# Performance work log

Hardware: AMD Instinct MI355X
Metric: run time of the kernel (lower is better)

The kernel has to match this reference:

```python
import jax, jax.numpy as jnp
import numpy as np

B, T, E = 8, 2048, 512   # batch, tokens, embedding_dim
K, C = 8192, 8           # num_embeddings, codebook_dim
LN_EPS = 1e-5


def _layer_norm(x, g, b):
    mu = jnp.mean(x, axis=-1, keepdims=True)
    var = jnp.var(x, axis=-1, keepdims=True)
    return (x - mu) * jax.lax.rsqrt(var + LN_EPS) * g + b


def setup_inputs() -> dict:
    key = jax.random.key(0)
    ks = jax.random.split(key, 8)
    s_e = 1.0 / np.sqrt(E)
    s_c = 1.0 / np.sqrt(C)
    return {
        "features": jax.random.normal(ks[0], (B, T, E), dtype=jnp.float32),
        # project_in: Linear(E,E) -> ReLU -> Linear(E,C)
        "W1_in": jax.random.uniform(ks[1], (E, E), jnp.float32, -s_e, s_e),
        "b1_in": jnp.zeros((E,), jnp.float32),
        "W2_in": jax.random.uniform(ks[2], (E, C), jnp.float32, -s_e, s_e),
        "b2_in": jnp.zeros((C,), jnp.float32),
        "ln_in_g": jnp.ones((C,), jnp.float32),
        "ln_in_b": jnp.zeros((C,), jnp.float32),
        # codebook
        "emb": jax.random.normal(ks[3], (K, C), dtype=jnp.float32),
        # project_out: Linear(C,E) -> ReLU -> Linear(E,E)
        "W1_out": jax.random.uniform(ks[4], (C, E), jnp.float32, -s_c, s_c),
        "b1_out": jnp.zeros((E,), jnp.float32),
        "W2_out": jax.random.uniform(ks[5], (E, E), jnp.float32, -s_e, s_e),
        "b2_out": jnp.zeros((E,), jnp.float32),
        "ln_out_g": jnp.ones((E,), jnp.float32),
        "ln_out_b": jnp.zeros((E,), jnp.float32),
    }


def reference(features, W1_in, b1_in, W2_in, b2_in, ln_in_g, ln_in_b, emb,
              W1_out, b1_out, W2_out, b2_out, ln_out_g, ln_out_b):
    # project_in + norm_in
    h = jax.nn.relu(jnp.einsum('bte,ef->btf', features, W1_in) + b1_in)
    z = jnp.einsum('bte,ec->btc', h, W2_in) + b2_in          # (B,T,C)
    z = _layer_norm(z, ln_in_g, ln_in_b)
    zf = z.reshape(-1, C)                                     # (N,C)
    d = (jnp.sum(zf * zf, axis=1, keepdims=True)
         - 2.0 * zf @ emb.T
         + jnp.sum(emb * emb, axis=1)[None, :])               # (N,K)
    idx = jnp.argmin(d, axis=1)                               # (N,)
    encodings = jax.nn.one_hot(idx, K, dtype=zf.dtype)        # (N,K)
    quantized = emb[idx]                                      # gather == one_hot @ emb
    # project_out + norm_out
    q = jax.nn.relu(quantized @ W1_out + b1_out)
    q = q @ W2_out + b2_out
    q = _layer_norm(q, ln_out_g, ln_out_b)
    q = q.reshape(B, T, E)
    return q, idx[:, None], encodings
```

## Files before the change

kernel.cpp:

```cpp
#include <hip/hip_runtime.h>
#include <cstdint>
#include <cstddef>

#define N_TOK 16384
#define E_DIM 512
#define C_DIM 8
#define K_CODES 8192
#define LN_EPS 1e-5f

template<bool RELU>
__global__ __launch_bounds__(256) void gemm_bias(const float* __restrict__ A,
    const float* __restrict__ B, const float* __restrict__ bias,
    float* __restrict__ C, int M, int N, int K) {
  __shared__ float As[16][132];
  __shared__ float Bs[16][68];
  const int tid = threadIdx.x;
  const int m0 = blockIdx.y * 128;
  const int n0 = blockIdx.x * 64;
  const int tx = tid & 15;
  const int ty = tid >> 4;
  const int ar = tid >> 1;
  const int ak = (tid & 1) * 8;
  const int bk = tid >> 4;
  const int bn = (tid & 15) * 4;
  float acc[8][4];
#pragma unroll
  for (int i = 0; i < 8; ++i)
#pragma unroll
    for (int j = 0; j < 4; ++j) acc[i][j] = 0.f;

  for (int k0 = 0; k0 < K; k0 += 16) {
    const float* Ap = A + (size_t)(m0 + ar) * K + (k0 + ak);
    float4 a0 = *(const float4*)(Ap);
    float4 a1 = *(const float4*)(Ap + 4);
    const float* Bp = B + (size_t)(k0 + bk) * N + (n0 + bn);
    float4 b0 = *(const float4*)(Bp);
    __syncthreads();
    As[ak + 0][ar] = a0.x; As[ak + 1][ar] = a0.y; As[ak + 2][ar] = a0.z; As[ak + 3][ar] = a0.w;
    As[ak + 4][ar] = a1.x; As[ak + 5][ar] = a1.y; As[ak + 6][ar] = a1.z; As[ak + 7][ar] = a1.w;
    Bs[bk][bn + 0] = b0.x; Bs[bk][bn + 1] = b0.y; Bs[bk][bn + 2] = b0.z; Bs[bk][bn + 3] = b0.w;
    __syncthreads();
#pragma unroll
    for (int kk = 0; kk < 16; ++kk) {
      float a[8], b[4];
#pragma unroll
      for (int i = 0; i < 8; ++i) a[i] = As[kk][ty * 8 + i];
#pragma unroll
      for (int j = 0; j < 4; ++j) b[j] = Bs[kk][tx * 4 + j];
#pragma unroll
      for (int i = 0; i < 8; ++i)
#pragma unroll
        for (int j = 0; j < 4; ++j) acc[i][j] = fmaf(a[i], b[j], acc[i][j]);
    }
  }
  float4 bv = *(const float4*)(bias + n0 + tx * 4);
#pragma unroll
  for (int i = 0; i < 8; ++i) {
    float4 r;
    r.x = acc[i][0] + bv.x; r.y = acc[i][1] + bv.y;
    r.z = acc[i][2] + bv.z; r.w = acc[i][3] + bv.w;
    if (RELU) {
      r.x = fmaxf(r.x, 0.f); r.y = fmaxf(r.y, 0.f);
      r.z = fmaxf(r.z, 0.f); r.w = fmaxf(r.w, 0.f);
    }
    *(float4*)(C + (size_t)(m0 + ty * 8 + i) * N + n0 + tx * 4) = r;
  }
}

__global__ __launch_bounds__(256) void zln_kernel(const float* __restrict__ h,
    const float* __restrict__ W2, const float* __restrict__ b2,
    const float* __restrict__ g, const float* __restrict__ b,
    float* __restrict__ z) {
  int token = blockIdx.x * 4 + (threadIdx.x >> 6);
  int lane = threadIdx.x & 63;
  const float* hr = h + (size_t)token * E_DIM;
  float acc[C_DIM];
#pragma unroll
  for (int c = 0; c < C_DIM; ++c) acc[c] = 0.f;
  for (int e = lane; e < E_DIM; e += 64) {
    float hv = hr[e];
    const float* w = W2 + e * C_DIM;
#pragma unroll
    for (int c = 0; c < C_DIM; ++c) acc[c] = fmaf(hv, w[c], acc[c]);
  }
#pragma unroll
  for (int c = 0; c < C_DIM; ++c) {
#pragma unroll
    for (int off = 32; off > 0; off >>= 1) acc[c] += __shfl_down(acc[c], off);
  }
  if (lane == 0) {
    float v[C_DIM]; float mu = 0.f;
#pragma unroll
    for (int c = 0; c < C_DIM; ++c) { v[c] = acc[c] + b2[c]; mu += v[c]; }
    mu *= 0.125f;
    float var = 0.f;
#pragma unroll
    for (int c = 0; c < C_DIM; ++c) { float d = v[c] - mu; var += d * d; }
    var *= 0.125f;
    float inv = 1.0f / sqrtf(var + LN_EPS);
#pragma unroll
    for (int c = 0; c < C_DIM; ++c)
      z[(size_t)token * C_DIM + c] = ((v[c] - mu) * inv) * g[c] + b[c];
  }
}

__global__ void ne_kernel(const float* __restrict__ emb, float* __restrict__ ne) {
  int k = blockIdx.x * 256 + threadIdx.x;
  const float* e = emb + (size_t)k * C_DIM;
  float s = 0.f;
#pragma unroll
  for (int c = 0; c < C_DIM; ++c) s = fmaf(e[c], e[c], s);
  ne[k] = s;
}

__global__ __launch_bounds__(256) void vq_partial(const float* __restrict__ z,
    const float* __restrict__ emb, const float* __restrict__ ne,
    float* __restrict__ pbest, int* __restrict__ pidx) {
  int chunk = blockIdx.x & 7;
  int token = (blockIdx.x >> 3) * 256 + threadIdx.x;
  float zv[C_DIM];
#pragma unroll
  for (int c = 0; c < C_DIM; ++c) zv[c] = z[(size_t)token * C_DIM + c];
  float s = 0.f;
#pragma unroll
  for (int c = 0; c < C_DIM; ++c) s = fmaf(zv[c], zv[c], s);
  float best = 3.402823466e38f; int bi = 0;
  int j0 = chunk * 1024;
  for (int j = j0; j < j0 + 1024; ++j) {
    const float* e = emb + (size_t)j * C_DIM;
    float p = 0.f;
#pragma unroll
    for (int c = 0; c < C_DIM; ++c) p = fmaf(zv[c], e[c], p);
    float d = fmaf(-2.f, p, s) + ne[j];
    if (d < best) { best = d; bi = j; }
  }
  pbest[chunk * N_TOK + token] = best;
  pidx[chunk * N_TOK + token] = bi;
}

__global__ void vq_combine(const float* __restrict__ pbest, const int* __restrict__ pidx,
    int* __restrict__ idx_i, float* __restrict__ idxf) {
  int n = blockIdx.x * 256 + threadIdx.x;
  float best = pbest[n]; int bi = pidx[n];
#pragma unroll
  for (int c = 1; c < 8; ++c) {
    float bb = pbest[c * N_TOK + n]; int i2 = pidx[c * N_TOK + n];
    if (bb < best) { best = bb; bi = i2; }
  }
  idx_i[n] = bi;
  idxf[n] = (float)bi;
}

__global__ __launch_bounds__(128) void proj_out1(const float* __restrict__ emb,
    const float* __restrict__ W1, const float* __restrict__ b1, float* __restrict__ t) {
  int k = blockIdx.x;
  int e = threadIdx.x * 4;
  float4 acc = *(const float4*)(b1 + e);
#pragma unroll
  for (int c = 0; c < C_DIM; ++c) {
    float ev = emb[(size_t)k * C_DIM + c];
    float4 w = *(const float4*)(W1 + (size_t)c * E_DIM + e);
    acc.x = fmaf(ev, w.x, acc.x); acc.y = fmaf(ev, w.y, acc.y);
    acc.z = fmaf(ev, w.z, acc.z); acc.w = fmaf(ev, w.w, acc.w);
  }
  acc.x = fmaxf(acc.x, 0.f); acc.y = fmaxf(acc.y, 0.f);
  acc.z = fmaxf(acc.z, 0.f); acc.w = fmaxf(acc.w, 0.f);
  *(float4*)(t + (size_t)k * E_DIM + e) = acc;
}

__global__ __launch_bounds__(256) void ln512(float* __restrict__ g,
    const float* __restrict__ gw, const float* __restrict__ bw) {
  int row = blockIdx.x; int tid = threadIdx.x;
  float* r = g + (size_t)row * E_DIM;
  float v0 = r[tid], v1 = r[tid + 256];
  __shared__ float red[8];
  int lane = tid & 63, wid = tid >> 6;
  float sum = v0 + v1;
#pragma unroll
  for (int off = 32; off > 0; off >>= 1) sum += __shfl_xor(sum, off);
  if (lane == 0) red[wid] = sum;
  __syncthreads();
  float mu = (red[0] + red[1] + red[2] + red[3]) * (1.0f / 512.0f);
  float d0 = v0 - mu, d1 = v1 - mu;
  float sq = d0 * d0 + d1 * d1;
#pragma unroll
  for (int off = 32; off > 0; off >>= 1) sq += __shfl_xor(sq, off);
  if (lane == 0) red[4 + wid] = sq;
  __syncthreads();
  float var = (red[4] + red[5] + red[6] + red[7]) * (1.0f / 512.0f);
  float inv = 1.0f / sqrtf(var + LN_EPS);
  r[tid]       = (d0 * inv) * gw[tid] + bw[tid];
  r[tid + 256] = (d1 * inv) * gw[tid + 256] + bw[tid + 256];
}

__global__ __launch_bounds__(128) void out_gather(const float* __restrict__ oc,
    const int* __restrict__ idx_i, float* __restrict__ q) {
  int n = blockIdx.x;
  int k = idx_i[n];
  int e = threadIdx.x * 4;
  *(float4*)(q + (size_t)n * E_DIM + e) = *(const float4*)(oc + (size_t)k * E_DIM + e);
}

__global__ void scatter_ones(const float* __restrict__ idxf, float* __restrict__ enc) {
  int n = blockIdx.x * 256 + threadIdx.x;
  int k = (int)idxf[n];
  enc[(size_t)n * K_CODES + k] = 1.0f;
}

extern "C" void kernel_launch(void* const* d_in, const int* in_sizes, int n_in,
                              void* d_out, int out_size, void* d_ws, size_t ws_size,
                              hipStream_t stream) {
  const float* features = (const float*)d_in[0];
  const float* W1_in  = (const float*)d_in[1];
  const float* b1_in  = (const float*)d_in[2];
  const float* W2_in  = (const float*)d_in[3];
  const float* b2_in  = (const float*)d_in[4];
  const float* ln_in_g = (const float*)d_in[5];
  const float* ln_in_b = (const float*)d_in[6];
  const float* emb    = (const float*)d_in[7];
  const float* W1_out = (const float*)d_in[8];
  const float* b1_out = (const float*)d_in[9];
  const float* W2_out = (const float*)d_in[10];
  const float* b2_out = (const float*)d_in[11];
  const float* ln_out_g = (const float*)d_in[12];
  const float* ln_out_b = (const float*)d_in[13];

  float* q    = (float*)d_out;
  float* idxf = q + (size_t)N_TOK * E_DIM;
  float* enc  = idxf + N_TOK;

  float* h     = enc;
  float* t     = enc + 8388608;
  float* g     = enc + 12582912;
  float* z     = enc + 16777216;
  float* ne    = enc + 16908288;
  float* pbest = enc + 16916480;
  int*   idx_i = (int*)(enc + 17047552);
  int*   pidx  = (int*)(enc + 17063936);

  ne_kernel<<<K_CODES / 256, 256, 0, stream>>>(emb, ne);

  dim3 g1(E_DIM / 64, N_TOK / 128);
  gemm_bias<true><<<g1, 256, 0, stream>>>(features, W1_in, b1_in, h, N_TOK, E_DIM, E_DIM);

  zln_kernel<<<N_TOK / 4, 256, 0, stream>>>(h, W2_in, b2_in, ln_in_g, ln_in_b, z);

  vq_partial<<<(N_TOK / 256) * 8, 256, 0, stream>>>(z, emb, ne, pbest, pidx);
  vq_combine<<<N_TOK / 256, 256, 0, stream>>>(pbest, pidx, idx_i, idxf);

  proj_out1<<<K_CODES, 128, 0, stream>>>(emb, W1_out, b1_out, t);

  dim3 g2(E_DIM / 64, K_CODES / 128);
  gemm_bias<false><<<g2, 256, 0, stream>>>(t, W2_out, b2_out, g, K_CODES, E_DIM, E_DIM);

  ln512<<<K_CODES, 256, 0, stream>>>(g, ln_out_g, ln_out_b);

  out_gather<<<N_TOK, 128, 0, stream>>>(g, idx_i, q);

  hipMemsetAsync(enc, 0, (size_t)N_TOK * K_CODES * sizeof(float), stream);
  scatter_ones<<<N_TOK / 256, 256, 0, stream>>>(idxf, enc);
}
```

Before: 882.2 us.

## Replace FP32 SIMT GEMMs with split-bf16 MFMA GEMMs using packed operands

```diff
diff --git a/kernel.cpp b/kernel.cpp
--- a/kernel.cpp
+++ b/kernel.cpp
@@ -8,62 +8,153 @@
 #define K_CODES 8192
 #define LN_EPS 1e-5f
 
+typedef __attribute__((ext_vector_type(8))) short short8;
+typedef __attribute__((ext_vector_type(4))) float f32x4;
+
+__device__ __forceinline__ unsigned short bf16_rn(float x) {
+  unsigned u = __float_as_uint(x);
+  unsigned r = u + 0x7FFFu + ((u >> 16) & 1u);
+  return (unsigned short)(r >> 16);
+}
+__device__ __forceinline__ float bf16_f(unsigned short h) {
+  return __uint_as_float(((unsigned)h) << 16);
+}
+
+__device__ __forceinline__ void gload16(const void* g, void* l) {
+  __builtin_amdgcn_global_load_lds(
+      (const __attribute__((address_space(1))) void*)g,
+      (__attribute__((address_space(3))) void*)l, 16, 0, 0);
+}
+
+__global__ __launch_bounds__(256) void pack_a(const float* __restrict__ A,
+    unsigned short* __restrict__ hi, unsigned short* __restrict__ lo) {
+  int t = blockIdx.x * 256 + threadIdx.x;
+  int l = t & 63;
+  int kt = (t >> 6) & 15;
+  int mf = t >> 10;
+  const float* src = A + (size_t)(mf * 16 + (l & 15)) * 512 + kt * 32 + (l >> 4) * 8;
+  float4 x0 = *(const float4*)src;
+  float4 x1 = *(const float4*)(src + 4);
+  float xs[8] = {x0.x, x0.y, x0.z, x0.w, x1.x, x1.y, x1.z, x1.w};
+  unsigned hw[4], lw[4];
+#pragma unroll
+  for (int p = 0; p < 4; ++p) {
+    float a = xs[2 * p], b = xs[2 * p + 1];
+    unsigned short ha = bf16_rn(a), hb = bf16_rn(b);
+    unsigned short la = bf16_rn(a - bf16_f(ha)), lb = bf16_rn(b - bf16_f(hb));
+    hw[p] = (unsigned)ha | ((unsigned)hb << 16);
+    lw[p] = (unsigned)la | ((unsigned)lb << 16);
+  }
+  uint4 hv; hv.x = hw[0]; hv.y = hw[1]; hv.z = hw[2]; hv.w = hw[3];
+  uint4 lv; lv.x = lw[0]; lv.y = lw[1]; lv.z = lw[2]; lv.w = lw[3];
+  ((uint4*)hi)[t] = hv;
+  ((uint4*)lo)[t] = lv;
+}
+
+__global__ __launch_bounds__(256) void pack_b(const float* __restrict__ B,
+    unsigned short* __restrict__ hi, unsigned short* __restrict__ lo) {
+  int t = blockIdx.x * 256 + threadIdx.x;
+  int l = t & 63;
+  int kt = (t >> 6) & 15;
+  int nf = t >> 10;
+  int col = nf * 16 + (l & 15);
+  int krow = kt * 32 + (l >> 4) * 8;
+  unsigned hw[4], lw[4];
+#pragma unroll
+  for (int p = 0; p < 4; ++p) {
+    float a = B[(size_t)(krow + 2 * p) * 512 + col];
+    float b = B[(size_t)(krow + 2 * p + 1) * 512 + col];
+    unsigned short ha = bf16_rn(a), hb = bf16_rn(b);
+    unsigned short la = bf16_rn(a - bf16_f(ha)), lb = bf16_rn(b - bf16_f(hb));
+    hw[p] = (unsigned)ha | ((unsigned)hb << 16);
+    lw[p] = (unsigned)la | ((unsigned)lb << 16);
+  }
+  uint4 hv; hv.x = hw[0]; hv.y = hw[1]; hv.z = hw[2]; hv.w = hw[3];
+  uint4 lv; lv.x = lw[0]; lv.y = lw[1]; lv.z = lw[2]; lv.w = lw[3];
+  ((uint4*)hi)[t] = hv;
+  ((uint4*)lo)[t] = lv;
+}
+
 template<bool RELU>
-__global__ __launch_bounds__(256) void gemm_bias(const float* __restrict__ A,
-    const float* __restrict__ B, const float* __restrict__ bias,
-    float* __restrict__ C, int M, int N, int K) {
-  __shared__ float As[16][132];
-  __shared__ float Bs[16][68];
+__global__ __launch_bounds__(256) void gemm_mfma(const unsigned short* __restrict__ Ah,
+    const unsigned short* __restrict__ Al, const unsigned short* __restrict__ Bh,
+    const unsigned short* __restrict__ Bl, const float* __restrict__ bias,
+    float* __restrict__ C) {
+  __shared__ char smem[32768];
   const int tid = threadIdx.x;
-  const int m0 = blockIdx.y * 128;
-  const int n0 = blockIdx.x * 64;
-  const int tx = tid & 15;
-  const int ty = tid >> 4;
-  const int ar = tid >> 1;
-  const int ak = (tid & 1) * 8;
-  const int bk = tid >> 4;
-  const int bn = (tid & 15) * 4;
-  float acc[8][4];
-#pragma unroll
-  for (int i = 0; i < 8; ++i)
-#pragma unroll
-    for (int j = 0; j < 4; ++j) acc[i][j] = 0.f;
-
-  for (int k0 = 0; k0 < K; k0 += 16) {
-    const float* Ap = A + (size_t)(m0 + ar) * K + (k0 + ak);
-    float4 a0 = *(const float4*)(Ap);
-    float4 a1 = *(const float4*)(Ap + 4);
-    const float* Bp = B + (size_t)(k0 + bk) * N + (n0 + bn);
-    float4 b0 = *(const float4*)(Bp);
+  const int l = tid & 63;
+  const int w = tid >> 6;
+  const int wm = w >> 1, wn = w & 1;
+  const int mblk = blockIdx.y, nblk = blockIdx.x;
+
+  char* sAh = smem;
+  char* sAl = smem + 8192;
+  char* sBh = smem + 16384;
+  char* sBl = smem + 24576;
+
+  const char* gAh = (const char*)Ah + (((size_t)(mblk * 8 + 2 * w) * 16) * 64 + l) * 16;
+  const char* gAl = (const char*)Al + (((size_t)(mblk * 8 + 2 * w) * 16) * 64 + l) * 16;
+  const char* gBh = (const char*)Bh + (((size_t)(nblk * 8 + 2 * w) * 16) * 64 + l) * 16;
+  const char* gBl = (const char*)Bl + (((size_t)(nblk * 8 + 2 * w) * 16) * 64 + l) * 16;
+  char* dA0 = sAh + (2 * w) * 1024;
+  char* dA1 = sAl + (2 * w) * 1024;
+  char* dB0 = sBh + (2 * w) * 1024;
+  char* dB1 = sBl + (2 * w) * 1024;
+
+  f32x4 acc[4][4];
+#pragma unroll
+  for (int i = 0; i < 4; ++i)
+#pragma unroll
+    for (int j = 0; j < 4; ++j) acc[i][j] = (f32x4){0.f, 0.f, 0.f, 0.f};
+
+  for (int kt = 0; kt < 16; ++kt) {
     __syncthreads();
-    As[ak + 0][ar] = a0.x; As[ak + 1][ar] = a0.y; As[ak + 2][ar] = a0.z; As[ak + 3][ar] = a0.w;
-    As[ak + 4][ar] = a1.x; As[ak + 5][ar] = a1.y; As[ak + 6][ar] = a1.z; As[ak + 7][ar] = a1.w;
-    Bs[bk][bn + 0] = b0.x; Bs[bk][bn + 1] = b0.y; Bs[bk][bn + 2] = b0.z; Bs[bk][bn + 3] = b0.w;
+    const size_t ko = (size_t)kt * 1024;
+    gload16(gAh + ko,           dA0);
+    gload16(gAh + ko + 16384,   dA0 + 1024);
+    gload16(gAl + ko,           dA1);
+    gload16(gAl + ko + 16384,   dA1 + 1024);
+    gload16(gBh + ko,           dB0);
+    gload16(gBh + ko + 16384,   dB0 + 1024);
+    gload16(gBl + ko,           dB1);
+    gload16(gBl + ko + 16384,   dB1 + 1024);
     __syncthreads();
-#pragma unroll
-    for (int kk = 0; kk < 16; ++kk) {
-      float a[8], b[4];
-#pragma unroll
-      for (int i = 0; i < 8; ++i) a[i] = As[kk][ty * 8 + i];
-#pragma unroll
-      for (int j = 0; j < 4; ++j) b[j] = Bs[kk][tx * 4 + j];
-#pragma unroll
-      for (int i = 0; i < 8; ++i)
-#pragma unroll
-        for (int j = 0; j < 4; ++j) acc[i][j] = fmaf(a[i], b[j], acc[i][j]);
+
+    short8 a_h[4], a_l[4], b_h[4], b_l[4];
+#pragma unroll
+    for (int i = 0; i < 4; ++i) {
+      a_h[i] = ((const short8*)sAh)[(wm * 4 + i) * 64 + l];
+      a_l[i] = ((const short8*)sAl)[(wm * 4 + i) * 64 + l];
     }
-  }
-  float4 bv = *(const float4*)(bias + n0 + tx * 4);
-#pragma unroll
-  for (int i = 0; i < 8; ++i) {
-    float4 r;
-    r.x = acc[i][0] + bv.x; r.y = acc[i][1] + bv.y;
-    r.z = acc[i][2] + bv.z; r.w = acc[i][3] + bv.w;
-    if (RELU) {
-      r.x = fmaxf(r.x, 0.f); r.y = fmaxf(r.y, 0.f);
-      r.z = fmaxf(r.z, 0.f); r.w = fmaxf(r.w, 0.f);
+#pragma unroll
+    for (int j = 0; j < 4; ++j) {
+      b_h[j] = ((const short8*)sBh)[(wn * 4 + j) * 64 + l];
+      b_l[j] = ((const short8*)sBl)[(wn * 4 + j) * 64 + l];
     }
-    *(float4*)(C + (size_t)(m0 + ty * 8 + i) * N + n0 + tx * 4) = r;
+#pragma unroll
+    for (int i = 0; i < 4; ++i)
+#pragma unroll
+      for (int j = 0; j < 4; ++j) {
+        acc[i][j] = __builtin_amdgcn_mfma_f32_16x16x32_bf16(a_h[i], b_h[j], acc[i][j], 0, 0, 0);
+        acc[i][j] = __builtin_amdgcn_mfma_f32_16x16x32_bf16(a_h[i], b_l[j], acc[i][j], 0, 0, 0);
+        acc[i][j] = __builtin_amdgcn_mfma_f32_16x16x32_bf16(a_l[i], b_h[j], acc[i][j], 0, 0, 0);
+      }
+  }
+
+  const int colb = nblk * 128 + wn * 64 + (l & 15);
+  const int rowb = mblk * 128 + wm * 64 + ((l >> 4) << 2);
+#pragma unroll
+  for (int j = 0; j < 4; ++j) {
+    float bv = bias[colb + j * 16];
+#pragma unroll
+    for (int i = 0; i < 4; ++i) {
+#pragma unroll
+      for (int r = 0; r < 4; ++r) {
+        float v = acc[i][j][r] + bv;
+        if (RELU) v = fmaxf(v, 0.f);
+        C[(size_t)(rowb + i * 16 + r) * 512 + colb + j * 16] = v;
+      }
+    }
   }
 }
 
@@ -237,11 +328,21 @@
   float* pbest = enc + 16916480;
   int*   idx_i = (int*)(enc + 17047552);
   int*   pidx  = (int*)(enc + 17063936);
+  unsigned short* A1h = (unsigned short*)(enc + 17195008);
+  unsigned short* A1l = (unsigned short*)(enc + 21389312);
+  unsigned short* A2h = (unsigned short*)(enc + 25583616);
+  unsigned short* A2l = (unsigned short*)(enc + 27680768);
+  unsigned short* B1h = (unsigned short*)(enc + 29777920);
+  unsigned short* B1l = (unsigned short*)(enc + 29908992);
+  unsigned short* B2h = (unsigned short*)(enc + 30040064);
+  unsigned short* B2l = (unsigned short*)(enc + 30171136);
 
   ne_kernel<<<K_CODES / 256, 256, 0, stream>>>(emb, ne);
 
-  dim3 g1(E_DIM / 64, N_TOK / 128);
-  gemm_bias<true><<<g1, 256, 0, stream>>>(features, W1_in, b1_in, h, N_TOK, E_DIM, E_DIM);
+  pack_b<<<128, 256, 0, stream>>>(W1_in, B1h, B1l);
+  pack_a<<<4096, 256, 0, stream>>>(features, A1h, A1l);
+  dim3 g1(4, N_TOK / 128);
+  gemm_mfma<true><<<g1, 256, 0, stream>>>(A1h, A1l, B1h, B1l, b1_in, h);
 
   zln_kernel<<<N_TOK / 4, 256, 0, stream>>>(h, W2_in, b2_in, ln_in_g, ln_in_b, z);
 
@@ -249,9 +350,10 @@
   vq_combine<<<N_TOK / 256, 256, 0, stream>>>(pbest, pidx, idx_i, idxf);
 
   proj_out1<<<K_CODES, 128, 0, stream>>>(emb, W1_out, b1_out, t);
-
-  dim3 g2(E_DIM / 64, K_CODES / 128);
-  gemm_bias<false><<<g2, 256, 0, stream>>>(t, W2_out, b2_out, g, K_CODES, E_DIM, E_DIM);
+  pack_b<<<128, 256, 0, stream>>>(W2_out, B2h, B2l);
+  pack_a<<<2048, 256, 0, stream>>>(t, A2h, A2l);
+  dim3 g2(4, K_CODES / 128);
+  gemm_mfma<false><<<g2, 256, 0, stream>>>(A2h, A2l, B2h, B2l, b2_out, g);
 
   ln512<<<K_CODES, 256, 0, stream>>>(g, ln_out_g, ln_out_b);
 
```

Result: faster. 793.8 us (-10.0%).
